# Performance work log

Hardware: AMD Instinct MI355X
Metric: run time of the kernel (lower is better)

## Reference

```python
import jax, jax.numpy as jnp
import numpy as np

B, TQ, TK, D = 16, 1024, 4096, 512


def setup_inputs() -> dict:
    key = jax.random.key(0)
    k1, k2, k3 = jax.random.split(key, 3)
    decoder_output = jax.random.normal(k1, (B, TQ, D), dtype=jnp.float32)
    encoder_output = jax.random.normal(k2, (B, TK, D), dtype=jnp.float32)
    # Keras Dense(lstm_size): kernel [D, D] (glorot-ish scale), bias [D] (zeros init)
    W_a = jax.random.normal(k3, (D, D), dtype=jnp.float32) * (1.0 / np.sqrt(D))
    b_a = jnp.zeros((D,), dtype=jnp.float32)
    return {"decoder_output": decoder_output, "encoder_output": encoder_output,
            "W_a": W_a, "b_a": b_a}


def reference(decoder_output, encoder_output, W_a, b_a):
    # Luong 'general' attention:
    # proj = Dense(encoder_output)            [B, Tk, D]
    proj = jnp.einsum('bkd,de->bke', encoder_output, W_a) + b_a
    # score = dec @ proj^T                    [B, Tq, Tk]
    score = jnp.einsum('bqd,bkd->bqk', decoder_output, proj)
    # softmax over encoder time axis (tf axis=2 == last axis here)
    alignment_vector = jax.nn.softmax(score, axis=-1)
    # context = align @ encoder_output        [B, Tq, D]
    context_vector = jnp.einsum('bqk,bkd->bqd', alignment_vector, encoder_output)
    return (context_vector, alignment_vector)
```

## Files before the change

### kernel.cpp

```cpp
#include <hip/hip_runtime.h>
#include <hip/hip_bf16.h>

#define B_  16
#define TQ_ 1024
#define TK_ 4096
#define D_  512

typedef unsigned short u16;
typedef __attribute__((ext_vector_type(8))) short short8;
typedef __attribute__((ext_vector_type(8))) _Float16 f16x8;
typedef __attribute__((ext_vector_type(4))) float f32x4;

__device__ __forceinline__ u16 bf16_rne(float x) {
  unsigned u = __float_as_uint(x);
  u += 0x7FFFu + ((u >> 16) & 1u);
  return (u16)(u >> 16);
}
__device__ __forceinline__ float bf16_as_f32(u16 h) {
  return __uint_as_float(((unsigned)h) << 16);
}
__device__ __forceinline__ void split_bf16(float x, u16& h, u16& l) {
  u16 hh = bf16_rne(x);
  h = hh;
  l = bf16_rne(x - bf16_as_f32(hh));
}

__device__ __forceinline__ void glld16(const void* g, void* lds) {
  __builtin_amdgcn_global_load_lds(
      (const __attribute__((address_space(1))) unsigned int*)g,
      (__attribute__((address_space(3))) unsigned int*)lds, 16, 0, 0);
}

__device__ __forceinline__ int seg_src4(int l) {
  return (l & 3) ^ ((l >> 2) & 3) ^ ((l >> 4) & 3);
}

__global__ __launch_bounds__(256) void transpose_conv_kernel(
    const float* __restrict__ E, _Float16* __restrict__ ET,
    _Float16* __restrict__ EF)
{
  __shared__ float tile[64][65];
  const int b  = blockIdx.z;
  const int k0 = blockIdx.x * 64;
  const int d0 = blockIdx.y * 64;
  const float* Eb = E + (long long)b * TK_ * D_;
  _Float16* ETb = ET + (long long)b * D_ * TK_;

  const int t  = threadIdx.x;
  const int r  = t >> 2;
  const int c4 = (t & 3) * 16;

  __align__(16) _Float16 g[16];
  #pragma unroll
  for (int i = 0; i < 16; i += 4) {
    float4 v = *(const float4*)&Eb[(long long)(k0 + r) * D_ + d0 + c4 + i];
    tile[r][c4 + i + 0] = v.x;
    tile[r][c4 + i + 1] = v.y;
    tile[r][c4 + i + 2] = v.z;
    tile[r][c4 + i + 3] = v.w;
    g[i + 0] = (_Float16)v.x;
    g[i + 1] = (_Float16)v.y;
    g[i + 2] = (_Float16)v.z;
    g[i + 3] = (_Float16)v.w;
  }
  if (EF) {
    _Float16* EFb = EF + (long long)b * TK_ * D_;
    uint4* dstF = (uint4*)&EFb[(long long)(k0 + r) * D_ + d0 + c4];
    dstF[0] = ((const uint4*)g)[0];
    dstF[1] = ((const uint4*)g)[1];
  }
  __syncthreads();

  __align__(16) _Float16 h[16];
  #pragma unroll
  for (int i = 0; i < 16; ++i) h[i] = (_Float16)tile[c4 + i][r];
  uint4* dst = (uint4*)&ETb[(long long)(d0 + r) * TK_ + k0 + c4];
  dst[0] = ((const uint4*)h)[0];
  dst[1] = ((const uint4*)h)[1];
}

#define DBM 128
#define DBN 128
#define DBK 32
#define DPAD 40

__global__ __launch_bounds__(256) void gemm_dec2_kernel(
    const float* __restrict__ A, const float* __restrict__ Bm,
    _Float16* __restrict__ Ch, _Float16* __restrict__ Cl)
{
  __shared__ u16 Ah[DBM * DPAD];
  __shared__ u16 Al[DBM * DPAD];
  __shared__ u16 Bh[DBN * DPAD];
  __shared__ u16 Bl[DBN * DPAD];

  const float* Ab = A  + (long long)(blockIdx.y * DBM) * D_;
  const float* Bb = Bm + (long long)(blockIdx.x * DBN) * D_;

  const int t    = threadIdx.x;
  const int r    = t >> 1;
  const int hf   = t & 1;
  const int lane = t & 63;
  const int wave = t >> 6;
  const int wr   = (wave >> 1) * 64;
  const int wc   = (wave & 1) * 64;
  const int ln   = lane & 15;
  const int qd   = lane >> 4;

  f32x4 acc[4][4];
  #pragma unroll
  for (int i = 0; i < 4; ++i)
    #pragma unroll
    for (int j = 0; j < 4; ++j) { f32x4 z = {0.f,0.f,0.f,0.f}; acc[i][j] = z; }

  const float* srcA = Ab + (long long)r * D_ + hf * 16;
  const float* srcB = Bb + (long long)r * D_ + hf * 16;
  u16* dAh = &Ah[r * DPAD + hf * 16];
  u16* dAl = &Al[r * DPAD + hf * 16];
  u16* dBh = &Bh[r * DPAD + hf * 16];
  u16* dBl = &Bl[r * DPAD + hf * 16];

  for (int k0 = 0; k0 < D_; k0 += DBK) {
    {
      __align__(16) u16 h[16], l[16];
      #pragma unroll
      for (int i = 0; i < 16; i += 4) {
        float4 v = *(const float4*)(srcA + k0 + i);
        split_bf16(v.x, h[i+0], l[i+0]);
        split_bf16(v.y, h[i+1], l[i+1]);
        split_bf16(v.z, h[i+2], l[i+2]);
        split_bf16(v.w, h[i+3], l[i+3]);
      }
      ((uint4*)dAh)[0] = ((const uint4*)h)[0];
      ((uint4*)dAh)[1] = ((const uint4*)h)[1];
      ((uint4*)dAl)[0] = ((const uint4*)l)[0];
      ((uint4*)dAl)[1] = ((const uint4*)l)[1];
      #pragma unroll
      for (int i = 0; i < 16; i += 4) {
        float4 v = *(const float4*)(srcB + k0 + i);
        split_bf16(v.x, h[i+0], l[i+0]);
        split_bf16(v.y, h[i+1], l[i+1]);
        split_bf16(v.z, h[i+2], l[i+2]);
        split_bf16(v.w, h[i+3], l[i+3]);
      }
      ((uint4*)dBh)[0] = ((const uint4*)h)[0];
      ((uint4*)dBh)[1] = ((const uint4*)h)[1];
      ((uint4*)dBl)[0] = ((const uint4*)l)[0];
      ((uint4*)dBl)[1] = ((const uint4*)l)[1];
    }
    __syncthreads();

    short8 fah[4], fal[4], fbh[4], fbl[4];
    #pragma unroll
    for (int i = 0; i < 4; ++i) {
      int ra = (wr + i * 16 + ln) * DPAD + qd * 8;
      int rb = (wc + i * 16 + ln) * DPAD + qd * 8;
      fah[i] = *(const short8*)&Ah[ra];
      fal[i] = *(const short8*)&Al[ra];
      fbh[i] = *(const short8*)&Bh[rb];
      fbl[i] = *(const short8*)&Bl[rb];
    }
    #pragma unroll
    for (int i = 0; i < 4; ++i)
      #pragma unroll
      for (int j = 0; j < 4; ++j) {
        acc[i][j] = __builtin_amdgcn_mfma_f32_16x16x32_bf16(fah[i], fbh[j], acc[i][j], 0, 0, 0);
        acc[i][j] = __builtin_amdgcn_mfma_f32_16x16x32_bf16(fah[i], fbl[j], acc[i][j], 0, 0, 0);
        acc[i][j] = __builtin_amdgcn_mfma_f32_16x16x32_bf16(fal[i], fbh[j], acc[i][j], 0, 0, 0);
      }
    __syncthreads();
  }

  const int m0 = blockIdx.y * DBM;
  const int n0 = blockIdx.x * DBN;
  #pragma unroll
  for (int i = 0; i < 4; ++i)
    #pragma unroll
    for (int j = 0; j < 4; ++j)
      #pragma unroll
      for (int rg = 0; rg < 4; ++rg) {
        int row = m0 + wr + i * 16 + qd * 4 + rg;
        int col = n0 + wc + j * 16 + ln;
        float x = acc[i][j][rg];
        _Float16 h = (_Float16)x;
        _Float16 l = (_Float16)(x - (float)h);
        long long idx = (long long)row * D_ + col;
        Ch[idx] = h;
        Cl[idx] = l;
      }
}

#define SBM 128
#define SBN 128
#define SBK 32
#define S_NT (D_ / SBK)

template<bool F16B>
__global__ __launch_bounds__(256) void gemm_score_kernel(
    const _Float16* __restrict__ A_h, const _Float16* __restrict__ A_l,
    const float* __restrict__ Bf, const _Float16* __restrict__ B16,
    float* __restrict__ C)
{
  __shared__ _Float16 sAh[3][SBM * SBK];
  __shared__ _Float16 sAl[3][SBM * SBK];
  __shared__ _Float16 sB [3][SBN * SBK];

  const int bz = blockIdx.z;
  const int m0 = blockIdx.y * SBM;
  const int n0 = blockIdx.x * SBN;
  const _Float16* Ahb = A_h + (long long)bz * TQ_ * D_ + (long long)m0 * D_;
  const _Float16* Alb = A_l + (long long)bz * TQ_ * D_ + (long long)m0 * D_;

  const int t    = threadIdx.x;
  const int lane = t & 63;
  const int wave = t >> 6;
  const int wr   = (wave >> 1) * 64;
  const int wc   = (wave & 1) * 64;
  const int ln   = lane & 15;
  const int qd   = lane >> 4;
  const int sw   = qd ^ (ln & 3) ^ (ln >> 2);

  f32x4 acc[4][4];
  #pragma unroll
  for (int i = 0; i < 4; ++i)
    #pragma unroll
    for (int j = 0; j < 4; ++j) { f32x4 z = {0.f,0.f,0.f,0.f}; acc[i][j] = z; }

  const int c0   = wave * 2;
  const int arow = c0 * 16 + (lane >> 2);
  const int ab   = seg_src4(lane) * 16;
  const char* gAh = (const char*)Ahb + (long long)arow * D_ * 2 + ab;
  const char* gAl = (const char*)Alb + (long long)arow * D_ * 2 + ab;
  const long long rstep = (long long)16 * D_ * 2;
  const int dstoff = c0 * 1024 + lane * 16;

  const char* gB16 = nullptr;
  if constexpr (F16B) {
    const _Float16* Bb16 = B16 + (long long)bz * TK_ * D_ + (long long)n0 * D_;
    gB16 = (const char*)Bb16 + (long long)arow * D_ * 2 + ab;
  }

  const float* Bb = Bf + (long long)bz * TK_ * D_ + (long long)n0 * D_;
  const int brow = t >> 1;
  const int bhf  = t & 1;
  const float* srcB = Bb + (long long)brow * D_ + bhf * 16;
  const int bh2 = (brow & 3) ^ ((brow >> 2) & 3);
  const int db0 = brow * SBK + ((2 * bhf    ) ^ bh2) * 8;
  const int db1 = brow * SBK + ((2 * bhf + 1) ^ bh2) * 8;

  auto stage = [&](int buf, int k0) {
    const long long ko = (long long)k0 * 2;
    char* dAh = (char*)sAh[buf] + dstoff;
    char* dAl = (char*)sAl[buf] + dstoff;
    glld16(gAh + ko, dAh);
    glld16(gAh + ko + rstep, dAh + 1024);
    glld16(gAl + ko, dAl);
    glld16(gAl + ko + rstep, dAl + 1024);
    if constexpr (F16B) {
      char* dBv = (char*)sB[buf] + dstoff;
      glld16(gB16 + ko, dBv);
      glld16(gB16 + ko + rstep, dBv + 1024);
    } else {
      __align__(16) _Float16 hb[16];
      #pragma unroll
      for (int i = 0; i < 16; i += 4) {
        float4 v = *(const float4*)(srcB + k0 + i);
        hb[i+0] = (_Float16)v.x;
        hb[i+1] = (_Float16)v.y;
        hb[i+2] = (_Float16)v.z;
        hb[i+3] = (_Float16)v.w;
      }
      *(uint4*)&sB[buf][db0] = ((const uint4*)hb)[0];
      *(uint4*)&sB[buf][db1] = ((const uint4*)hb)[1];
    }
  };

  stage(0, 0);
  stage(1, SBK);
  if constexpr (F16B) {
    asm volatile("s_waitcnt vmcnt(6)" ::: "memory");
  } else {
    asm volatile("s_waitcnt vmcnt(0) lgkmcnt(0)" ::: "memory");
  }
  __builtin_amdgcn_s_barrier();
  __builtin_amdgcn_sched_barrier(0);

  #pragma unroll
  for (int tt = 0; tt < S_NT; ++tt) {
    const int cur = tt % 3;
    const int nxt = (tt + 2) % 3;
    if (tt + 2 < S_NT) stage(nxt, (tt + 2) * SBK);

    const _Float16* bAh = sAh[cur];
    const _Float16* bAl = sAl[cur];
    const _Float16* bBv = sB[cur];
    f16x8 fah[4], fal[4], fb[4];
    #pragma unroll
    for (int i = 0; i < 4; ++i) {
      const int ra = (wr + i * 16 + ln) * SBK + sw * 8;
      const int rb = (wc + i * 16 + ln) * SBK + sw * 8;
      fah[i] = *(const f16x8*)&bAh[ra];
      fal[i] = *(const f16x8*)&bAl[ra];
      fb[i]  = *(const f16x8*)&bBv[rb];
    }
    __builtin_amdgcn_s_setprio(1);
    #pragma unroll
    for (int i = 0; i < 4; ++i)
      #pragma unroll
      for (int j = 0; j < 4; ++j) {
        acc[i][j] = __builtin_amdgcn_mfma_f32_16x16x32_f16(fah[i], fb[j], acc[i][j], 0, 0, 0);
        acc[i][j] = __builtin_amdgcn_mfma_f32_16x16x32_f16(fal[i], fb[j], acc[i][j], 0, 0, 0);
      }
    __builtin_amdgcn_s_setprio(0);
    if (tt + 1 < S_NT) {
      if constexpr (F16B) {
        if (tt + 2 < S_NT) {
          asm volatile("s_waitcnt vmcnt(6)" ::: "memory");
        } else {
          asm volatile("s_waitcnt vmcnt(0)" ::: "memory");
        }
      } else {
        asm volatile("s_waitcnt vmcnt(0) lgkmcnt(0)" ::: "memory");
      }
      __builtin_amdgcn_s_barrier();
      __builtin_amdgcn_sched_barrier(0);
    }
  }

  float* Cb = C + (long long)bz * TQ_ * TK_;
  #pragma unroll
  for (int i = 0; i < 4; ++i)
    #pragma unroll
    for (int j = 0; j < 4; ++j)
      #pragma unroll
      for (int rg = 0; rg < 4; ++rg) {
        int row = m0 + wr + i * 16 + qd * 4 + rg;
        int col = n0 + wc + j * 16 + ln;
        Cb[(long long)row * TK_ + col] = acc[i][j][rg];
      }
}

template<bool WP16>
__global__ __launch_bounds__(256) void softmax_kernel(
    float* __restrict__ P, _Float16* __restrict__ P16)
{
  __shared__ float red[8];
  float* p = P + (long long)blockIdx.x * TK_;
  const int t    = threadIdx.x;
  const int lane = t & 63;
  const int wave = t >> 6;

  float4 v[4];
  float mx = -3.0e38f;
  #pragma unroll
  for (int i = 0; i < 4; ++i) {
    v[i] = *(const float4*)&p[i * 1024 + t * 4];
    mx = fmaxf(mx, fmaxf(fmaxf(v[i].x, v[i].y), fmaxf(v[i].z, v[i].w)));
  }
  #pragma unroll
  for (int o = 32; o > 0; o >>= 1) mx = fmaxf(mx, __shfl_xor(mx, o, 64));
  if (lane == 0) red[wave] = mx;
  __syncthreads();
  mx = fmaxf(fmaxf(red[0], red[1]), fmaxf(red[2], red[3]));

  float s = 0.f;
  #pragma unroll
  for (int i = 0; i < 4; ++i) {
    v[i].x = __expf(v[i].x - mx);
    v[i].y = __expf(v[i].y - mx);
    v[i].z = __expf(v[i].z - mx);
    v[i].w = __expf(v[i].w - mx);
    s += (v[i].x + v[i].y) + (v[i].z + v[i].w);
  }
  #pragma unroll
  for (int o = 32; o > 0; o >>= 1) s += __shfl_xor(s, o, 64);
  if (lane == 0) red[4 + wave] = s;
  __syncthreads();
  s = (red[4] + red[5]) + (red[6] + red[7]);
  const float inv = 1.0f / s;

  _Float16* p16 = WP16 ? (P16 + (long long)blockIdx.x * TK_) : nullptr;
  #pragma unroll
  for (int i = 0; i < 4; ++i) {
    v[i].x *= inv; v[i].y *= inv; v[i].z *= inv; v[i].w *= inv;
    *(float4*)&p[i * 1024 + t * 4] = v[i];
    if constexpr (WP16) {
      union { _Float16 h[4]; uint2 u; } pk;
      pk.h[0] = (_Float16)v[i].x;
      pk.h[1] = (_Float16)v[i].y;
      pk.h[2] = (_Float16)v[i].z;
      pk.h[3] = (_Float16)v[i].w;
      *(uint2*)&p16[i * 1024 + t * 4] = pk.u;
    }
  }
}

#define CBM 64
#define CBN 128
#define CBK 32
#define C_NT (TK_ / CBK)

template<bool F16A>
__global__ __launch_bounds__(256) void gemm_ctx_kernel(
    const float* __restrict__ P, const _Float16* __restrict__ P16,
    const _Float16* __restrict__ ET, float* __restrict__ C)
{
  __shared__ _Float16 sA[3][CBM * CBK];
  __shared__ _Float16 sB[3][CBN * CBK];

  const int bid = blockIdx.x;
  const int s   = (bid & 7) * 128 + (bid >> 3);
  const int m0  = (s & 15) * CBM;
  const int n0  = ((s >> 4) & 3) * CBN;
  const int bz  = s >> 6;

  const float*    Pb = P  + (long long)bz * TQ_ * TK_ + (long long)m0 * TK_;
  const _Float16* Eb = ET + (long long)bz * D_ * TK_  + (long long)n0 * TK_;

  const int t    = threadIdx.x;
  const int lane = t & 63;
  const int wave = t >> 6;
  const int wr   = (wave >> 1) * 32;
  const int wc   = (wave & 1) * 64;
  const int ln   = lane & 15;
  const int qd   = lane >> 4;
  const int sw   = qd ^ (ln & 3) ^ (ln >> 2);

  f32x4 acc[2][4];
  #pragma unroll
  for (int i = 0; i < 2; ++i)
    #pragma unroll
    for (int j = 0; j < 4; ++j) { f32x4 z = {0.f,0.f,0.f,0.f}; acc[i][j] = z; }

  const int ab = seg_src4(lane) * 16;
  const char* gB = (const char*)Eb + ((long long)(wave * 32 + (lane >> 2)) * TK_) * 2 + ab;
  const long long rstepB = (long long)16 * TK_ * 2;
  const int bdst = wave * 2048 + lane * 16;
  const char* gA16 = nullptr;
  if constexpr (F16A) {
    const _Float16* Pb16 = P16 + (long long)bz * TQ_ * TK_ + (long long)m0 * TK_;
    gA16 = (const char*)Pb16 + ((long long)(wave * 16 + (lane >> 2)) * TK_) * 2 + ab;
  }
  const int adst = wave * 1024 + lane * 16;

  const int arowf = t >> 2;
  const int asegf = t & 3;
  const float* gAf = Pb + (long long)arowf * TK_ + asegf * 8;
  const int afoff = arowf * CBK + ((asegf ^ (arowf & 3) ^ ((arowf >> 2) & 3)) * 8);

  auto stage = [&](int buf, int k0) {
    const long long ko = (long long)k0 * 2;
    char* dB = (char*)sB[buf] + bdst;
    glld16(gB + ko, dB);
    glld16(gB + ko + rstepB, dB + 1024);
    if constexpr (F16A) {
      glld16(gA16 + ko, (char*)sA[buf] + adst);
    } else {
      float4 v0 = *(const float4*)(gAf + k0);
      float4 v1 = *(const float4*)(gAf + k0 + 4);
      __align__(16) _Float16 hb[8];
      hb[0] = (_Float16)v0.x; hb[1] = (_Float16)v0.y;
      hb[2] = (_Float16)v0.z; hb[3] = (_Float16)v0.w;
      hb[4] = (_Float16)v1.x; hb[5] = (_Float16)v1.y;
      hb[6] = (_Float16)v1.z; hb[7] = (_Float16)v1.w;
      *(uint4*)&sA[buf][afoff] = *(const uint4*)hb;
    }
  };

  stage(0, 0);
  stage(1, CBK);
  if constexpr (F16A) {
    asm volatile("s_waitcnt vmcnt(3)" ::: "memory");
  } else {
    asm volatile("s_waitcnt vmcnt(0) lgkmcnt(0)" ::: "memory");
  }
  __builtin_amdgcn_s_barrier();
  __builtin_amdgcn_sched_barrier(0);

  int cur = 0, nxt = 2;
  #pragma unroll 1
  for (int tt = 0; tt < C_NT; ++tt) {
    if (tt + 2 < C_NT) stage(nxt, (tt + 2) * CBK);

    const _Float16* bA  = sA[cur];
    const _Float16* bBv = sB[cur];
    f16x8 fa[2], fb[4];
    #pragma unroll
    for (int i = 0; i < 2; ++i)
      fa[i] = *(const f16x8*)&bA[(wr + i * 16 + ln) * CBK + sw * 8];
    #pragma unroll
    for (int j = 0; j < 4; ++j)
      fb[j] = *(const f16x8*)&bBv[(wc + j * 16 + ln) * CBK + sw * 8];
    __builtin_amdgcn_s_setprio(1);
    #pragma unroll
    for (int i = 0; i < 2; ++i)
      #pragma unroll
      for (int j = 0; j < 4; ++j)
        acc[i][j] = __builtin_amdgcn_mfma_f32_16x16x32_f16(fa[i], fb[j], acc[i][j], 0, 0, 0);
    __builtin_amdgcn_s_setprio(0);
    if (tt + 1 < C_NT) {
      if constexpr (F16A) {
        if (tt + 2 < C_NT) {
          asm volatile("s_waitcnt vmcnt(3)" ::: "memory");
        } else {
          asm volatile("s_waitcnt vmcnt(0)" ::: "memory");
        }
      } else {
        asm volatile("s_waitcnt vmcnt(0) lgkmcnt(0)" ::: "memory");
      }
      __builtin_amdgcn_s_barrier();
      __builtin_amdgcn_sched_barrier(0);
    }
    cur = (cur == 2) ? 0 : cur + 1;
    nxt = (nxt == 2) ? 0 : nxt + 1;
  }

  float* Cb = C + (long long)bz * TQ_ * D_;
  #pragma unroll
  for (int i = 0; i < 2; ++i)
    #pragma unroll
    for (int j = 0; j < 4; ++j)
      #pragma unroll
      for (int rg = 0; rg < 4; ++rg) {
        int row = m0 + wr + i * 16 + qd * 4 + rg;
        int col = n0 + wc + j * 16 + ln;
        Cb[(long long)row * D_ + col] = acc[i][j][rg];
      }
}

extern "C" void kernel_launch(void* const* d_in, const int* in_sizes, int n_in,
                              void* d_out, int out_size, void* d_ws, size_t ws_size,
                              hipStream_t stream) {
  (void)in_sizes; (void)n_in; (void)out_size;
  const float* dec = (const float*)d_in[0];
  const float* enc = (const float*)d_in[1];
  const float* Wa  = (const float*)d_in[2];

  float* ctx   = (float*)d_out;
  float* align = ctx + (long long)B_ * TQ_ * D_;

  char* ws = (char*)d_ws;
  const size_t SZ_ENCT = (size_t)B_ * D_ * TK_ * 2;
  const size_t SZ_DEC2 = (size_t)B_ * TQ_ * D_ * 2;
  const size_t SZ_ENCF = (size_t)B_ * TK_ * D_ * 2;
  const size_t SZ_P16  = (size_t)B_ * TQ_ * TK_ * 2;

  _Float16* encT  = (_Float16*)(ws);
  _Float16* dec2h = (_Float16*)(ws + SZ_ENCT);
  _Float16* dec2l = (_Float16*)(ws + SZ_ENCT + SZ_DEC2);
  _Float16* encF  = (_Float16*)(ws + SZ_ENCT + 2 * SZ_DEC2);
  _Float16* p16   = (_Float16*)(ws + SZ_ENCT);

  const bool mid  = ws_size >= SZ_ENCT + 2 * SZ_DEC2 + SZ_ENCF;
  const bool full = ws_size >= SZ_ENCT + SZ_P16;

  transpose_conv_kernel<<<dim3(TK_ / 64, D_ / 64, B_), 256, 0, stream>>>(
      enc, encT, mid ? encF : nullptr);

  gemm_dec2_kernel<<<dim3(D_ / DBN, (B_ * TQ_) / DBM, 1), 256, 0, stream>>>(
      dec, Wa, dec2h, dec2l);

  if (mid)
    gemm_score_kernel<true><<<dim3(TK_ / SBN, TQ_ / SBM, B_), 256, 0, stream>>>(
        dec2h, dec2l, enc, encF, align);
  else
    gemm_score_kernel<false><<<dim3(TK_ / SBN, TQ_ / SBM, B_), 256, 0, stream>>>(
        dec2h, dec2l, enc, nullptr, align);

  if (full)
    softmax_kernel<true><<<B_ * TQ_, 256, 0, stream>>>(align, p16);
  else
    softmax_kernel<false><<<B_ * TQ_, 256, 0, stream>>>(align, nullptr);

  if (full)
    gemm_ctx_kernel<true><<<dim3((TQ_ / CBM) * (D_ / CBN) * B_), 256, 0, stream>>>(
        align, p16, encT, ctx);
  else
    gemm_ctx_kernel<false><<<dim3((TQ_ / CBM) * (D_ / CBN) * B_), 256, 0, stream>>>(
        align, nullptr, encT, ctx);
}
```

Before: 868.8 us.

## Pre-split dec and W into bf16 planes and simplify score GEMM buffering

```diff
diff --git a/kernel.cpp b/kernel.cpp
--- a/kernel.cpp
+++ b/kernel.cpp
@@ -33,6 +33,27 @@
 
 __device__ __forceinline__ int seg_src4(int l) {
   return (l & 3) ^ ((l >> 2) & 3) ^ ((l >> 4) & 3);
+}
+
+__global__ __launch_bounds__(256) void split_planes_kernel(
+    const float* __restrict__ X, u16* __restrict__ H, u16* __restrict__ L,
+    int n8)
+{
+  int i = blockIdx.x * 256 + threadIdx.x;
+  if (i >= n8) return;
+  const float4* src = (const float4*)X + (size_t)i * 2;
+  float4 a = src[0], b = src[1];
+  __align__(16) u16 h[8], l[8];
+  split_bf16(a.x, h[0], l[0]);
+  split_bf16(a.y, h[1], l[1]);
+  split_bf16(a.z, h[2], l[2]);
+  split_bf16(a.w, h[3], l[3]);
+  split_bf16(b.x, h[4], l[4]);
+  split_bf16(b.y, h[5], l[5]);
+  split_bf16(b.z, h[6], l[6]);
+  split_bf16(b.w, h[7], l[7]);
+  *(uint4*)&H[(size_t)i * 8] = *(const uint4*)h;
+  *(uint4*)&L[(size_t)i * 8] = *(const uint4*)l;
 }
 
 __global__ __launch_bounds__(256) void transpose_conv_kernel(
@@ -79,6 +100,98 @@
   dst[1] = ((const uint4*)h)[1];
 }
 
+#define D2BM 64
+#define D2BN 128
+#define D2BK 32
+
+__global__ __launch_bounds__(256) void gemm_dec2p_kernel(
+    const u16* __restrict__ Ahp, const u16* __restrict__ Alp,
+    const u16* __restrict__ Bhp, const u16* __restrict__ Blp,
+    _Float16* __restrict__ Ch, _Float16* __restrict__ Cl)
+{
+  __shared__ u16 sAh[D2BM * D2BK];
+  __shared__ u16 sAl[D2BM * D2BK];
+  __shared__ u16 sBh[D2BN * D2BK];
+  __shared__ u16 sBl[D2BN * D2BK];
+
+  const int m0 = blockIdx.y * D2BM;
+  const int n0 = blockIdx.x * D2BN;
+
+  const int t    = threadIdx.x;
+  const int lane = t & 63;
+  const int wave = t >> 6;
+  const int wrm  = (wave >> 1) * 32;
+  const int wcn  = (wave & 1) * 64;
+  const int ln   = lane & 15;
+  const int qd   = lane >> 4;
+  const int sw   = qd ^ (ln & 3) ^ (ln >> 2);
+
+  f32x4 acc[2][4];
+  #pragma unroll
+  for (int i = 0; i < 2; ++i)
+    #pragma unroll
+    for (int j = 0; j < 4; ++j) { f32x4 z = {0.f,0.f,0.f,0.f}; acc[i][j] = z; }
+
+  const int ab = seg_src4(lane) * 16;
+  const char* gAh = (const char*)Ahp + (long long)(m0 + wave * 16 + (lane >> 2)) * D_ * 2 + ab;
+  const char* gAl = (const char*)Alp + (long long)(m0 + wave * 16 + (lane >> 2)) * D_ * 2 + ab;
+  const int adst = wave * 1024 + lane * 16;
+  const char* gBh = (const char*)Bhp + (long long)(n0 + wave * 32 + (lane >> 2)) * D_ * 2 + ab;
+  const char* gBl = (const char*)Blp + (long long)(n0 + wave * 32 + (lane >> 2)) * D_ * 2 + ab;
+  const long long rstep = (long long)16 * D_ * 2;
+  const int bdst = wave * 2048 + lane * 16;
+
+  for (int k0 = 0; k0 < D_; k0 += D2BK) {
+    const long long ko = (long long)k0 * 2;
+    glld16(gAh + ko, (char*)sAh + adst);
+    glld16(gAl + ko, (char*)sAl + adst);
+    glld16(gBh + ko, (char*)sBh + bdst);
+    glld16(gBh + ko + rstep, (char*)sBh + bdst + 1024);
+    glld16(gBl + ko, (char*)sBl + bdst);
+    glld16(gBl + ko + rstep, (char*)sBl + bdst + 1024);
+    __syncthreads();
+
+    short8 fah[2], fal[2], fbh[4], fbl[4];
+    #pragma unroll
+    for (int i = 0; i < 2; ++i) {
+      const int ra = (wrm + i * 16 + ln) * D2BK + sw * 8;
+      fah[i] = *(const short8*)&sAh[ra];
+      fal[i] = *(const short8*)&sAl[ra];
+    }
+    #pragma unroll
+    for (int j = 0; j < 4; ++j) {
+      const int rb = (wcn + j * 16 + ln) * D2BK + sw * 8;
+      fbh[j] = *(const short8*)&sBh[rb];
+      fbl[j] = *(const short8*)&sBl[rb];
+    }
+    #pragma unroll
+    for (int i = 0; i < 2; ++i)
+      #pragma unroll
+      for (int j = 0; j < 4; ++j) {
+        acc[i][j] = __builtin_amdgcn_mfma_f32_16x16x32_bf16(fah[i], fbh[j], acc[i][j], 0, 0, 0);
+        acc[i][j] = __builtin_amdgcn_mfma_f32_16x16x32_bf16(fah[i], fbl[j], acc[i][j], 0, 0, 0);
+        acc[i][j] = __builtin_amdgcn_mfma_f32_16x16x32_bf16(fal[i], fbh[j], acc[i][j], 0, 0, 0);
+      }
+    __syncthreads();
+  }
+
+  #pragma unroll
+  for (int i = 0; i < 2; ++i)
+    #pragma unroll
+    for (int j = 0; j < 4; ++j)
+      #pragma unroll
+      for (int rg = 0; rg < 4; ++rg) {
+        int row = m0 + wrm + i * 16 + qd * 4 + rg;
+        int col = n0 + wcn + j * 16 + ln;
+        float x = acc[i][j][rg];
+        _Float16 h = (_Float16)x;
+        _Float16 l = (_Float16)(x - (float)h);
+        long long idx = (long long)row * D_ + col;
+        Ch[idx] = h;
+        Cl[idx] = l;
+      }
+}
+
 #define DBM 128
 #define DBN 128
 #define DBK 32
@@ -192,7 +305,6 @@
 #define SBM 128
 #define SBN 128
 #define SBK 32
-#define S_NT (D_ / SBK)
 
 template<bool F16B>
 __global__ __launch_bounds__(256) void gemm_score_kernel(
@@ -200,9 +312,9 @@
     const float* __restrict__ Bf, const _Float16* __restrict__ B16,
     float* __restrict__ C)
 {
-  __shared__ _Float16 sAh[3][SBM * SBK];
-  __shared__ _Float16 sAl[3][SBM * SBK];
-  __shared__ _Float16 sB [3][SBN * SBK];
+  __shared__ _Float16 sAh[SBM * SBK];
+  __shared__ _Float16 sAl[SBM * SBK];
+  __shared__ _Float16 sB [SBN * SBK];
 
   const int bz = blockIdx.z;
   const int m0 = blockIdx.y * SBM;
@@ -231,7 +343,9 @@
   const char* gAh = (const char*)Ahb + (long long)arow * D_ * 2 + ab;
   const char* gAl = (const char*)Alb + (long long)arow * D_ * 2 + ab;
   const long long rstep = (long long)16 * D_ * 2;
-  const int dstoff = c0 * 1024 + lane * 16;
+  char* lAh = (char*)sAh + c0 * 1024 + lane * 16;
+  char* lAl = (char*)sAl + c0 * 1024 + lane * 16;
+  char* lB  = (char*)sB  + c0 * 1024 + lane * 16;
 
   const char* gB16 = nullptr;
   if constexpr (F16B) {
@@ -244,21 +358,17 @@
   const int bhf  = t & 1;
   const float* srcB = Bb + (long long)brow * D_ + bhf * 16;
   const int bh2 = (brow & 3) ^ ((brow >> 2) & 3);
-  const int db0 = brow * SBK + ((2 * bhf    ) ^ bh2) * 8;
-  const int db1 = brow * SBK + ((2 * bhf + 1) ^ bh2) * 8;
-
-  auto stage = [&](int buf, int k0) {
-    const long long ko = (long long)k0 * 2;
-    char* dAh = (char*)sAh[buf] + dstoff;
-    char* dAl = (char*)sAl[buf] + dstoff;
-    glld16(gAh + ko, dAh);
-    glld16(gAh + ko + rstep, dAh + 1024);
-    glld16(gAl + ko, dAl);
-    glld16(gAl + ko + rstep, dAl + 1024);
+  _Float16* dB0 = &sB[brow * SBK + ((2 * bhf    ) ^ bh2) * 8];
+  _Float16* dB1 = &sB[brow * SBK + ((2 * bhf + 1) ^ bh2) * 8];
+
+  for (int k0 = 0; k0 < D_; k0 += SBK) {
+    glld16(gAh + (long long)k0 * 2, lAh);
+    glld16(gAh + (long long)k0 * 2 + rstep, lAh + 1024);
+    glld16(gAl + (long long)k0 * 2, lAl);
+    glld16(gAl + (long long)k0 * 2 + rstep, lAl + 1024);
     if constexpr (F16B) {
-      char* dBv = (char*)sB[buf] + dstoff;
-      glld16(gB16 + ko, dBv);
-      glld16(gB16 + ko + rstep, dBv + 1024);
+      glld16(gB16 + (long long)k0 * 2, lB);
+      glld16(gB16 + (long long)k0 * 2 + rstep, lB + 1024);
     } else {
       __align__(16) _Float16 hb[16];
       #pragma unroll
@@ -269,40 +379,20 @@
         hb[i+2] = (_Float16)v.z;
         hb[i+3] = (_Float16)v.w;
       }
-      *(uint4*)&sB[buf][db0] = ((const uint4*)hb)[0];
-      *(uint4*)&sB[buf][db1] = ((const uint4*)hb)[1];
-    }
-  };
-
-  stage(0, 0);
-  stage(1, SBK);
-  if constexpr (F16B) {
-    asm volatile("s_waitcnt vmcnt(6)" ::: "memory");
-  } else {
-    asm volatile("s_waitcnt vmcnt(0) lgkmcnt(0)" ::: "memory");
-  }
-  __builtin_amdgcn_s_barrier();
-  __builtin_amdgcn_sched_barrier(0);
-
-  #pragma unroll
-  for (int tt = 0; tt < S_NT; ++tt) {
-    const int cur = tt % 3;
-    const int nxt = (tt + 2) % 3;
-    if (tt + 2 < S_NT) stage(nxt, (tt + 2) * SBK);
-
-    const _Float16* bAh = sAh[cur];
-    const _Float16* bAl = sAl[cur];
-    const _Float16* bBv = sB[cur];
+      *(uint4*)dB0 = ((const uint4*)hb)[0];
+      *(uint4*)dB1 = ((const uint4*)hb)[1];
+    }
+    __syncthreads();
+
     f16x8 fah[4], fal[4], fb[4];
     #pragma unroll
     for (int i = 0; i < 4; ++i) {
-      const int ra = (wr + i * 16 + ln) * SBK + sw * 8;
-      const int rb = (wc + i * 16 + ln) * SBK + sw * 8;
-      fah[i] = *(const f16x8*)&bAh[ra];
-      fal[i] = *(const f16x8*)&bAl[ra];
-      fb[i]  = *(const f16x8*)&bBv[rb];
-    }
-    __builtin_amdgcn_s_setprio(1);
+      int ra = (wr + i * 16 + ln) * SBK + sw * 8;
+      int rb = (wc + i * 16 + ln) * SBK + sw * 8;
+      fah[i] = *(const f16x8*)&sAh[ra];
+      fal[i] = *(const f16x8*)&sAl[ra];
+      fb[i]  = *(const f16x8*)&sB[rb];
+    }
     #pragma unroll
     for (int i = 0; i < 4; ++i)
       #pragma unroll
@@ -310,20 +400,7 @@
         acc[i][j] = __builtin_amdgcn_mfma_f32_16x16x32_f16(fah[i], fb[j], acc[i][j], 0, 0, 0);
         acc[i][j] = __builtin_amdgcn_mfma_f32_16x16x32_f16(fal[i], fb[j], acc[i][j], 0, 0, 0);
       }
-    __builtin_amdgcn_s_setprio(0);
-    if (tt + 1 < S_NT) {
-      if constexpr (F16B) {
-        if (tt + 2 < S_NT) {
-          asm volatile("s_waitcnt vmcnt(6)" ::: "memory");
-        } else {
-          asm volatile("s_waitcnt vmcnt(0)" ::: "memory");
-        }
-      } else {
-        asm volatile("s_waitcnt vmcnt(0) lgkmcnt(0)" ::: "memory");
-      }
-      __builtin_amdgcn_s_barrier();
-      __builtin_amdgcn_sched_barrier(0);
-    }
+    __syncthreads();
   }
 
   float* Cb = C + (long long)bz * TQ_ * TK_;
@@ -543,21 +620,36 @@
   const size_t SZ_DEC2 = (size_t)B_ * TQ_ * D_ * 2;
   const size_t SZ_ENCF = (size_t)B_ * TK_ * D_ * 2;
   const size_t SZ_P16  = (size_t)B_ * TQ_ * TK_ * 2;
+  const size_t SZ_WB   = (size_t)D_ * D_ * 2;
 
   _Float16* encT  = (_Float16*)(ws);
   _Float16* dec2h = (_Float16*)(ws + SZ_ENCT);
   _Float16* dec2l = (_Float16*)(ws + SZ_ENCT + SZ_DEC2);
   _Float16* encF  = (_Float16*)(ws + SZ_ENCT + 2 * SZ_DEC2);
   _Float16* p16   = (_Float16*)(ws + SZ_ENCT);
+  u16* dech = (u16*)(ws + SZ_ENCT + SZ_P16);
+  u16* decl = dech + (size_t)B_ * TQ_ * D_;
+  u16* Wh   = decl + (size_t)B_ * TQ_ * D_;
+  u16* Wl   = Wh + (size_t)D_ * D_;
 
   const bool mid  = ws_size >= SZ_ENCT + 2 * SZ_DEC2 + SZ_ENCF;
   const bool full = ws_size >= SZ_ENCT + SZ_P16;
+  const bool pre  = ws_size >= SZ_ENCT + SZ_P16 + 2 * SZ_DEC2 + 2 * SZ_WB;
 
   transpose_conv_kernel<<<dim3(TK_ / 64, D_ / 64, B_), 256, 0, stream>>>(
       enc, encT, mid ? encF : nullptr);
 
-  gemm_dec2_kernel<<<dim3(D_ / DBN, (B_ * TQ_) / DBM, 1), 256, 0, stream>>>(
-      dec, Wa, dec2h, dec2l);
+  if (pre) {
+    split_planes_kernel<<<dim3((B_ * TQ_ * D_ / 8) / 256), 256, 0, stream>>>(
+        dec, dech, decl, B_ * TQ_ * D_ / 8);
+    split_planes_kernel<<<dim3((D_ * D_ / 8) / 256), 256, 0, stream>>>(
+        Wa, Wh, Wl, D_ * D_ / 8);
+    gemm_dec2p_kernel<<<dim3(D_ / D2BN, (B_ * TQ_) / D2BM), 256, 0, stream>>>(
+        dech, decl, Wh, Wl, dec2h, dec2l);
+  } else {
+    gemm_dec2_kernel<<<dim3(D_ / DBN, (B_ * TQ_) / DBM), 256, 0, stream>>>(
+        dec, Wa, dec2h, dec2l);
+  }
 
   if (mid)
     gemm_score_kernel<true><<<dim3(TK_ / SBN, TQ_ / SBM, B_), 256, 0, stream>>>(
```

Result: no change. 853.0 us (-1.8%).
